# Optimization experiments

Measured on AMD Instinct MI355X. Metric: run time of the kernel, lower is better.

## Reference

```python
import jax, jax.numpy as jnp
import numpy as np

N_NODES = 50000
N_EDGES = 640000
IN_DIM = 4
EMBED = 128
OUT_DIM = 1
N_LAYERS = 3


def setup_inputs() -> dict:
    key = jax.random.key(0)
    ks = jax.random.split(key, 12)
    node_feats = jax.random.normal(ks[0], (N_NODES, IN_DIM), dtype=jnp.float32)
    src = jax.random.randint(ks[1], (N_EDGES,), 0, N_NODES, dtype=jnp.int64 if jax.config.x64_enabled else jnp.int32)
    dst = jax.random.randint(ks[2], (N_EDGES,), 0, N_NODES, dtype=jnp.int64 if jax.config.x64_enabled else jnp.int32)
    s = 1.0 / np.sqrt(EMBED)
    W_emb = jax.random.normal(ks[3], (IN_DIM, EMBED), dtype=jnp.float32) * (1.0 / np.sqrt(IN_DIM))
    b_emb = jnp.zeros((EMBED,), dtype=jnp.float32)
    W_g = jax.random.normal(ks[4], (N_LAYERS, EMBED, EMBED), dtype=jnp.float32) * s
    b_g = jnp.zeros((N_LAYERS, EMBED), dtype=jnp.float32)
    W_o1 = jax.random.normal(ks[5], (EMBED, EMBED), dtype=jnp.float32) * s
    b_o1 = jnp.zeros((EMBED,), dtype=jnp.float32)
    W_o2 = jax.random.normal(ks[6], (EMBED, OUT_DIM), dtype=jnp.float32) * s
    b_o2 = jnp.zeros((OUT_DIM,), dtype=jnp.float32)
    return {"node_feats": node_feats, "src": src, "dst": dst,
            "W_emb": W_emb, "b_emb": b_emb, "W_g": W_g, "b_g": b_g,
            "W_o1": W_o1, "b_o1": b_o1, "W_o2": W_o2, "b_o2": b_o2}


def reference(node_feats, src, dst, W_emb, b_emb, W_g, b_g, W_o1, b_o1, W_o2, b_o2):
    n = node_feats.shape[0]
    ones = jnp.ones(src.shape[0], dtype=node_feats.dtype)
    # DGL GraphConv norm='both': symmetric degree normalization, degrees clamped to >=1
    out_deg = jnp.clip(jax.ops.segment_sum(ones, src, num_segments=n), 1.0)
    in_deg = jnp.clip(jax.ops.segment_sum(ones, dst, num_segments=n), 1.0)
    norm_src = (out_deg ** -0.5)[:, None]  # [N,1]
    norm_dst = (in_deg ** -0.5)[:, None]   # [N,1]

    h = node_feats @ W_emb + b_emb  # [N, E]
    for l in range(W_g.shape[0]):
        x = h * norm_src                                        # scale sources
        agg = jax.ops.segment_sum(x[src], dst, num_segments=n)  # SpMM gather/scatter
        h = agg * norm_dst
        h = h @ W_g[l] + b_g[l]
        h = jax.nn.relu(h)
    h = jax.nn.relu(h @ W_o1 + b_o1)
    return h @ W_o2 + b_o2  # [N, out_dim]
```

## Files before the change

kernel.cpp:

```cpp
#include <hip/hip_runtime.h>

#define NN 50000
#define NE 640000
#define NPAD 50176
#define SCAN_B 196

typedef short bf16x8 __attribute__((ext_vector_type(8)));
typedef float f32x4 __attribute__((ext_vector_type(4)));

__device__ __forceinline__ unsigned short f2bf(float f) {
  unsigned int u = __float_as_uint(f);
  unsigned int r = (u + 0x7FFFu + ((u >> 16) & 1u)) >> 16;
  return (unsigned short)r;
}
__device__ __forceinline__ float bf2f(unsigned short h) {
  return __uint_as_float(((unsigned int)h) << 16);
}

typedef const __attribute__((address_space(1))) void* gptr_t;
typedef __attribute__((address_space(3))) void* lptr_t;
__device__ __forceinline__ void gload16(const void* g, void* l) {
  __builtin_amdgcn_global_load_lds((gptr_t)g, (lptr_t)l, 16, 0, 0);
}

__global__ __launch_bounds__(256) void k_deg(const int* __restrict__ src,
                                             const int* __restrict__ dst,
                                             int* __restrict__ rep_out,
                                             int* __restrict__ rep_in,
                                             int* __restrict__ rank) {
  int e = blockIdx.x * 256 + threadIdx.x;
  int r = blockIdx.x & 7;
  if (e < NE) {
    atomicAdd(&rep_out[r * NPAD + src[e]], 1);
    rank[e] = atomicAdd(&rep_in[r * NPAD + dst[e]], 1);
  }
}

__global__ __launch_bounds__(256) void k_scan1(const int* __restrict__ rep_out,
                                               const int* __restrict__ rep_in,
                                               float* __restrict__ nsrc,
                                               float* __restrict__ ndst,
                                               int* __restrict__ in_cnt,
                                               int* __restrict__ repoff,
                                               int* __restrict__ bsum) {
  int t = threadIdx.x, n = blockIdx.x * 256 + t;
  int tot_in = 0;
  if (n < NN) {
    int od = 0;
#pragma unroll
    for (int r = 0; r < 8; ++r) od += rep_out[r * NPAD + n];
    int pf = 0;
#pragma unroll
    for (int r = 0; r < 8; ++r) {
      repoff[n * 8 + r] = pf;
      pf += rep_in[r * NPAD + n];
    }
    tot_in = pf;
    in_cnt[n] = tot_in;
    nsrc[n] = 1.0f / sqrtf((float)max(od, 1));
    ndst[n] = 1.0f / sqrtf((float)max(tot_in, 1));
  }
  int s = tot_in;
#pragma unroll
  for (int o = 32; o >= 1; o >>= 1) s += __shfl_down(s, o);
  __shared__ int ws4[4];
  if ((t & 63) == 0) ws4[t >> 6] = s;
  __syncthreads();
  if (t == 0) bsum[blockIdx.x] = ws4[0] + ws4[1] + ws4[2] + ws4[3];
}

__global__ __launch_bounds__(256) void k_scan3(const int* __restrict__ in_cnt,
                                               const int* __restrict__ bsum,
                                               int* __restrict__ row_start) {
  int b = blockIdx.x, t = threadIdx.x, lane = t & 63, w = t >> 6;
  __shared__ int wtot[4];
  __shared__ int sbase;
  {
    int v = (t < b) ? bsum[t] : 0;
#pragma unroll
    for (int o = 32; o >= 1; o >>= 1) v += __shfl_down(v, o);
    if (lane == 0) wtot[w] = v;
    __syncthreads();
    if (t == 0) sbase = wtot[0] + wtot[1] + wtot[2] + wtot[3];
    __syncthreads();
  }
  int i = b * 256 + t;
  int v = (i < NN) ? in_cnt[i] : 0;
  int sc = v;
#pragma unroll
  for (int o = 1; o < 64; o <<= 1) {
    int x = __shfl_up(sc, o);
    if (lane >= o) sc += x;
  }
  if (lane == 63) wtot[w] = sc;
  __syncthreads();
  int base = sbase;
  for (int j = 0; j < w; ++j) base += wtot[j];
  if (i < NN) row_start[i] = base + sc - v;
}

__global__ __launch_bounds__(256) void k_fill(const int* __restrict__ src,
                                              const int* __restrict__ dst,
                                              const int* __restrict__ row_start,
                                              const int* __restrict__ repoff,
                                              const int* __restrict__ rank,
                                              int* __restrict__ col) {
  int e = blockIdx.x * 256 + threadIdx.x;
  int r = blockIdx.x & 7;
  if (e < NE) {
    int d = dst[e];
    col[row_start[d] + repoff[d * 8 + r] + rank[e]] = src[e];
  }
}

__global__ __launch_bounds__(256) void k_embed_prep(const float* __restrict__ nf,
                                                    const float* __restrict__ W,
                                                    const float* __restrict__ b,
                                                    const float* __restrict__ nsrc,
                                                    float* __restrict__ xs,
                                                    const float* __restrict__ Wg,
                                                    const float* __restrict__ Wo1,
                                                    unsigned short* __restrict__ wt) {
  int bid = blockIdx.x;
  if (bid < 25000) {
    int idx = bid * 256 + threadIdx.x;
    int n = idx >> 7, j = idx & 127;
    const float* f = nf + n * 4;
    float acc = b[j];
    acc += f[0] * W[j] + f[1] * W[128 + j] + f[2] * W[256 + j] + f[3] * W[384 + j];
    xs[idx] = acc * nsrc[n];
  } else {
    int idx = (bid - 25000) * 256 + threadIdx.x;
    int mat = idx >> 14, rem = idx & 16383;
    int k = rem >> 7, n = rem & 127;
    const float* Wsrc = (mat < 3) ? (Wg + mat * 16384) : Wo1;
    float v = Wsrc[k * 128 + n];
    unsigned short hi = f2bf(v);
    float lo = v - bf2f(hi);
    unsigned short* base = wt + mat * 32768;
    base[n * 128 + k] = hi;
    base[16384 + n * 128 + k] = f2bf(lo);
  }
}

__global__ __launch_bounds__(256) void k_spmm(const float* __restrict__ xs,
                                              unsigned short* __restrict__ ahi,
                                              unsigned short* __restrict__ alo,
                                              const int* __restrict__ col,
                                              const int* __restrict__ row_start,
                                              const int* __restrict__ in_cnt,
                                              const float* __restrict__ ndst) {
  int node = blockIdx.x * 4 + (threadIdx.x >> 6);
  int lane = threadIdx.x & 63;
  int half = lane >> 5;
  int ql = lane & 31;
  int start = row_start[node];
  int cnt = in_cnt[node];
  float4 acc = make_float4(0.f, 0.f, 0.f, 0.f);
  const float4* X4 = (const float4*)xs;
  for (int base = 0; base < cnt; base += 64) {
    int m = min(cnt - base, 64);
    int ccol = (lane < m) ? col[start + base + lane] : 0;
    for (int jj = 0; jj < m; jj += 8) {
      int i0 = jj + half, i1 = i0 + 2, i2 = i0 + 4, i3 = i0 + 6;
      int mm = m - 1;
      int s0 = __shfl(ccol, min(i0, mm));
      int s1 = __shfl(ccol, min(i1, mm));
      int s2 = __shfl(ccol, min(i2, mm));
      int s3 = __shfl(ccol, min(i3, mm));
      float f0 = (i0 < m) ? 1.f : 0.f;
      float f1 = (i1 < m) ? 1.f : 0.f;
      float f2 = (i2 < m) ? 1.f : 0.f;
      float f3 = (i3 < m) ? 1.f : 0.f;
      float4 v0 = X4[(size_t)s0 * 32 + ql];
      float4 v1 = X4[(size_t)s1 * 32 + ql];
      float4 v2 = X4[(size_t)s2 * 32 + ql];
      float4 v3 = X4[(size_t)s3 * 32 + ql];
      acc.x = fmaf(f0, v0.x, acc.x); acc.y = fmaf(f0, v0.y, acc.y);
      acc.z = fmaf(f0, v0.z, acc.z); acc.w = fmaf(f0, v0.w, acc.w);
      acc.x = fmaf(f1, v1.x, acc.x); acc.y = fmaf(f1, v1.y, acc.y);
      acc.z = fmaf(f1, v1.z, acc.z); acc.w = fmaf(f1, v1.w, acc.w);
      acc.x = fmaf(f2, v2.x, acc.x); acc.y = fmaf(f2, v2.y, acc.y);
      acc.z = fmaf(f2, v2.z, acc.z); acc.w = fmaf(f2, v2.w, acc.w);
      acc.x = fmaf(f3, v3.x, acc.x); acc.y = fmaf(f3, v3.y, acc.y);
      acc.z = fmaf(f3, v3.z, acc.z); acc.w = fmaf(f3, v3.w, acc.w);
    }
  }
  acc.x += __shfl_down(acc.x, 32);
  acc.y += __shfl_down(acc.y, 32);
  acc.z += __shfl_down(acc.z, 32);
  acc.w += __shfl_down(acc.w, 32);
  if (half == 0) {
    float nd = ndst[node];
    float v0 = acc.x * nd, v1 = acc.y * nd, v2 = acc.z * nd, v3 = acc.w * nd;
    ushort4 h, l;
    h.x = f2bf(v0); l.x = f2bf(v0 - bf2f(h.x));
    h.y = f2bf(v1); l.y = f2bf(v1 - bf2f(h.y));
    h.z = f2bf(v2); l.z = f2bf(v2 - bf2f(h.z));
    h.w = f2bf(v3); l.w = f2bf(v3 - bf2f(h.w));
    *(ushort4*)(ahi + (size_t)node * 128 + ql * 4) = h;
    *(ushort4*)(alo + (size_t)node * 128 + ql * 4) = l;
  }
}

__global__ __launch_bounds__(256) void k_gemm_mfma(
    const unsigned short* __restrict__ Ahi, const unsigned short* __restrict__ Alo,
    const unsigned short* __restrict__ Wth, const unsigned short* __restrict__ Wtl,
    const float* __restrict__ bias, float* __restrict__ outf,
    unsigned short* __restrict__ outhi, unsigned short* __restrict__ outlo,
    const float* __restrict__ nsrc, const float* __restrict__ W_o2,
    const float* __restrict__ b_o2, int M, int mode) {
  __shared__ unsigned short sm[2 * 64 * 128];
  __shared__ float smred[4][64];
  int tid = threadIdx.x;
  int lane = tid & 63, w = tid >> 6;
  int tile0 = blockIdx.x * 64;

  {
    int slot = lane & 15;
#pragma unroll
    for (int j = 0; j < 4; ++j) {
      int ldsoff = w * 4096 + j * 1024;
      int row = (ldsoff >> 8) + (lane >> 4);
      int grow = tile0 + row;
      if (grow > M - 1) grow = M - 1;
      size_t gsrc = (size_t)grow * 256 + (size_t)(((slot ^ (row & 7)) << 4));
      gload16((const char*)Ahi + gsrc, (char*)sm + ldsoff);
      gload16((const char*)Alo + gsrc, (char*)sm + 16384 + ldsoff);
    }
  }

  bf16x8 bh[2][4], bl[2][4];
  {
    int koff = (lane >> 4) * 8;
#pragma unroll
    for (int cf = 0; cf < 2; ++cf) {
      int n = w * 32 + cf * 16 + (lane & 15);
      const unsigned short* ph = Wth + (size_t)n * 128 + koff;
      const unsigned short* pl = Wtl + (size_t)n * 128 + koff;
#pragma unroll
      for (int kc = 0; kc < 4; ++kc) {
        bh[cf][kc] = *(const bf16x8*)(ph + kc * 32);
        bl[cf][kc] = *(const bf16x8*)(pl + kc * 32);
      }
    }
  }

  f32x4 acc[4][2] = {};
  __syncthreads();

  int r15 = lane & 15, kq = lane >> 4;
  for (int kc = 0; kc < 4; ++kc) {
    bf16x8 ah[4], al[4];
#pragma unroll
    for (int m = 0; m < 4; ++m) {
      int row = m * 16 + r15;
      int boff = row * 256 + ((((kc * 4 + kq) ^ (row & 7))) << 4);
      ah[m] = *(const bf16x8*)((const char*)sm + boff);
      al[m] = *(const bf16x8*)((const char*)sm + 16384 + boff);
    }
#pragma unroll
    for (int m = 0; m < 4; ++m)
#pragma unroll
      for (int cf = 0; cf < 2; ++cf) {
        acc[m][cf] = __builtin_amdgcn_mfma_f32_16x16x32_bf16(ah[m], bh[cf][kc], acc[m][cf], 0, 0, 0);
        acc[m][cf] = __builtin_amdgcn_mfma_f32_16x16x32_bf16(ah[m], bl[cf][kc], acc[m][cf], 0, 0, 0);
        acc[m][cf] = __builtin_amdgcn_mfma_f32_16x16x32_bf16(al[m], bh[cf][kc], acc[m][cf], 0, 0, 0);
      }
  }

  if (mode == 3) {
    float w2v[2], bv2[2];
#pragma unroll
    for (int cf = 0; cf < 2; ++cf) {
      int colg = w * 32 + cf * 16 + r15;
      w2v[cf] = W_o2[colg];
      bv2[cf] = bias[colg];
    }
#pragma unroll
    for (int m = 0; m < 4; ++m) {
#pragma unroll
      for (int i = 0; i < 4; ++i) {
        float p = fmaxf(acc[m][0][i] + bv2[0], 0.f) * w2v[0] +
                  fmaxf(acc[m][1][i] + bv2[1], 0.f) * w2v[1];
#pragma unroll
        for (int msk = 1; msk < 16; msk <<= 1) p += __shfl_xor(p, msk);
        if (r15 == 0) smred[w][m * 16 + kq * 4 + i] = p;
      }
    }
    __syncthreads();
    if (tid < 64) {
      int gr = tile0 + tid;
      if (gr < M)
        outf[gr] = smred[0][tid] + smred[1][tid] + smred[2][tid] + smred[3][tid] + b_o2[0];
    }
    return;
  }
#pragma unroll
  for (int cf = 0; cf < 2; ++cf) {
    int colg = w * 32 + cf * 16 + r15;
    float bv = bias[colg];
#pragma unroll
    for (int m = 0; m < 4; ++m) {
#pragma unroll
      for (int i = 0; i < 4; ++i) {
        int gr = tile0 + m * 16 + kq * 4 + i;
        if (gr < M) {
          float v = fmaxf(acc[m][cf][i] + bv, 0.f);
          if (mode == 0) {
            outf[(size_t)gr * 128 + colg] = v * nsrc[gr];
          } else {
            unsigned short h = f2bf(v);
            outhi[(size_t)gr * 128 + colg] = h;
            outlo[(size_t)gr * 128 + colg] = f2bf(v - bf2f(h));
          }
        }
      }
    }
  }
}

extern "C" void kernel_launch(void* const* d_in, const int* in_sizes, int n_in,
                              void* d_out, int out_size, void* d_ws, size_t ws_size,
                              hipStream_t stream) {
  const float* node_feats = (const float*)d_in[0];
  const int* src = (const int*)d_in[1];
  const int* dst = (const int*)d_in[2];
  const float* W_emb = (const float*)d_in[3];
  const float* b_emb = (const float*)d_in[4];
  const float* W_g = (const float*)d_in[5];
  const float* b_g = (const float*)d_in[6];
  const float* W_o1 = (const float*)d_in[7];
  const float* b_o1 = (const float*)d_in[8];
  const float* W_o2 = (const float*)d_in[9];
  const float* b_o2 = (const float*)d_in[10];
  float* out = (float*)d_out;

  char* ws = (char*)d_ws;
  int* rep_out   = (int*)(ws + 0);
  int* rep_in    = (int*)(ws + 1605632);
  int* in_cnt    = (int*)(ws + 3211264);
  int* row_start = (int*)(ws + 3411968);
  float* nsrc    = (float*)(ws + 3612672);
  float* ndst    = (float*)(ws + 3813376);
  int* repoff    = (int*)(ws + 4014080);
  int* bsum      = (int*)(ws + 5619712);
  int* col       = (int*)(ws + 5620736);
  unsigned short* wt = (unsigned short*)(ws + 8180736);
  float* X       = (float*)(ws + 8442880);
  unsigned short* Xu = (unsigned short*)(ws + 8442880);
  int* rank      = (int*)(ws + 8442880);
  unsigned short* Ahi = (unsigned short*)(ws + 34042880);
  unsigned short* Alo = (unsigned short*)(ws + 46842880);

  hipMemsetAsync(d_ws, 0, 3211264, stream);

  k_deg<<<(NE + 255) / 256, 256, 0, stream>>>(src, dst, rep_out, rep_in, rank);
  k_scan1<<<SCAN_B, 256, 0, stream>>>(rep_out, rep_in, nsrc, ndst, in_cnt, repoff, bsum);
  k_scan3<<<SCAN_B, 256, 0, stream>>>(in_cnt, bsum, row_start);
  k_fill<<<(NE + 255) / 256, 256, 0, stream>>>(src, dst, row_start, repoff, rank, col);
  k_embed_prep<<<25256, 256, 0, stream>>>(node_feats, W_emb, b_emb, nsrc, X,
                                          W_g, W_o1, wt);

  int gemm_grid = (NN + 63) / 64;
  for (int l = 0; l < 3; ++l) {
    k_spmm<<<NN / 4, 256, 0, stream>>>(X, Ahi, Alo, col, row_start, in_cnt, ndst);
    unsigned short* wth = wt + l * 32768;
    unsigned short* wtl = wth + 16384;
    if (l < 2) {
      k_gemm_mfma<<<gemm_grid, 256, 0, stream>>>(Ahi, Alo, wth, wtl, b_g + l * 128,
                                                 X, nullptr, nullptr, nsrc,
                                                 nullptr, nullptr, NN, 0);
    } else {
      k_gemm_mfma<<<gemm_grid, 256, 0, stream>>>(Ahi, Alo, wth, wtl, b_g + l * 128,
                                                 nullptr, Xu, Xu + 6400000, nsrc,
                                                 nullptr, nullptr, NN, 1);
    }
  }
  k_gemm_mfma<<<gemm_grid, 256, 0, stream>>>(Xu, Xu + 6400000, wt + 3 * 32768,
                                             wt + 3 * 32768 + 16384, b_o1,
                                             out, nullptr, nullptr, nsrc,
                                             W_o2, b_o2, NN, 3);
}
```

Baseline: 390.1 us.

## Build CSR with per-block LDS histograms instead of global atomics

```diff
diff --git a/kernel.cpp b/kernel.cpp
--- a/kernel.cpp
+++ b/kernel.cpp
@@ -4,6 +4,10 @@
 #define NE 640000
 #define NPAD 50176
 #define SCAN_B 196
+#define OUT_CHUNKS 64
+#define OUT_CE 10000
+#define IN_CHUNKS 128
+#define IN_CE 5000
 
 typedef short bf16x8 __attribute__((ext_vector_type(8)));
 typedef float f32x4 __attribute__((ext_vector_type(4)));
@@ -23,37 +27,52 @@
   __builtin_amdgcn_global_load_lds((gptr_t)g, (lptr_t)l, 16, 0, 0);
 }
 
-__global__ __launch_bounds__(256) void k_deg(const int* __restrict__ src,
-                                             const int* __restrict__ dst,
-                                             int* __restrict__ rep_out,
-                                             int* __restrict__ rep_in,
-                                             int* __restrict__ rank) {
-  int e = blockIdx.x * 256 + threadIdx.x;
-  int r = blockIdx.x & 7;
-  if (e < NE) {
-    atomicAdd(&rep_out[r * NPAD + src[e]], 1);
-    rank[e] = atomicAdd(&rep_in[r * NPAD + dst[e]], 1);
-  }
-}
-
-__global__ __launch_bounds__(256) void k_scan1(const int* __restrict__ rep_out,
-                                               const int* __restrict__ rep_in,
+__global__ __launch_bounds__(256) void k_hist(const int* __restrict__ src,
+                                              const int* __restrict__ dst,
+                                              unsigned short* __restrict__ hist_out,
+                                              unsigned short* __restrict__ hist_in) {
+  __shared__ unsigned int h[NPAD / 2];
+  int b = blockIdx.x, tid = threadIdx.x;
+  for (int i = tid; i < NPAD / 2; i += 256) h[i] = 0;
+  __syncthreads();
+  if (b < OUT_CHUNKS) {
+    int base = b * OUT_CE;
+    for (int i = tid; i < OUT_CE; i += 256) {
+      int n = src[base + i];
+      atomicAdd(&h[n >> 1], (n & 1) ? 0x10000u : 1u);
+    }
+  } else {
+    int base = (b - OUT_CHUNKS) * IN_CE;
+    for (int i = tid; i < IN_CE; i += 256) {
+      int n = dst[base + i];
+      atomicAdd(&h[n >> 1], (n & 1) ? 0x10000u : 1u);
+    }
+  }
+  __syncthreads();
+  unsigned int* outp = (unsigned int*)((b < OUT_CHUNKS ? hist_out : hist_in) +
+                                       (size_t)(b < OUT_CHUNKS ? b : b - OUT_CHUNKS) * NPAD);
+  for (int i = tid; i < NPAD / 2; i += 256) outp[i] = h[i];
+}
+
+__global__ __launch_bounds__(256) void k_scan1(const unsigned short* __restrict__ hist_out,
+                                               unsigned short* __restrict__ hist_in,
                                                float* __restrict__ nsrc,
                                                float* __restrict__ ndst,
                                                int* __restrict__ in_cnt,
-                                               int* __restrict__ repoff,
                                                int* __restrict__ bsum) {
   int t = threadIdx.x, n = blockIdx.x * 256 + t;
   int tot_in = 0;
   if (n < NN) {
     int od = 0;
-#pragma unroll
-    for (int r = 0; r < 8; ++r) od += rep_out[r * NPAD + n];
+#pragma unroll 8
+    for (int c = 0; c < OUT_CHUNKS; ++c) od += hist_out[(size_t)c * NPAD + n];
     int pf = 0;
-#pragma unroll
-    for (int r = 0; r < 8; ++r) {
-      repoff[n * 8 + r] = pf;
-      pf += rep_in[r * NPAD + n];
+#pragma unroll 8
+    for (int c = 0; c < IN_CHUNKS; ++c) {
+      size_t idx = (size_t)c * NPAD + n;
+      unsigned short v = hist_in[idx];
+      hist_in[idx] = (unsigned short)pf;
+      pf += v;
     }
     tot_in = pf;
     in_cnt[n] = tot_in;
@@ -102,14 +121,18 @@
 __global__ __launch_bounds__(256) void k_fill(const int* __restrict__ src,
                                               const int* __restrict__ dst,
                                               const int* __restrict__ row_start,
-                                              const int* __restrict__ repoff,
-                                              const int* __restrict__ rank,
+                                              const unsigned short* __restrict__ prefix,
                                               int* __restrict__ col) {
-  int e = blockIdx.x * 256 + threadIdx.x;
-  int r = blockIdx.x & 7;
-  if (e < NE) {
-    int d = dst[e];
-    col[row_start[d] + repoff[d * 8 + r] + rank[e]] = src[e];
+  __shared__ unsigned int h[NPAD / 2];
+  int c = blockIdx.x, tid = threadIdx.x;
+  for (int i = tid; i < NPAD / 2; i += 256) h[i] = 0;
+  __syncthreads();
+  int base = c * IN_CE;
+  for (int i = tid; i < IN_CE; i += 256) {
+    int d = dst[base + i];
+    unsigned int old = atomicAdd(&h[d >> 1], (d & 1) ? 0x10000u : 1u);
+    int rank = (d & 1) ? (int)(old >> 16) : (int)(old & 0xFFFFu);
+    col[row_start[d] + (int)prefix[(size_t)c * NPAD + d] + rank] = src[base + i];
   }
 }
 
@@ -137,9 +160,9 @@
     float v = Wsrc[k * 128 + n];
     unsigned short hi = f2bf(v);
     float lo = v - bf2f(hi);
-    unsigned short* base = wt + mat * 32768;
-    base[n * 128 + k] = hi;
-    base[16384 + n * 128 + k] = f2bf(lo);
+    unsigned short* basep = wt + mat * 32768;
+    basep[n * 128 + k] = hi;
+    basep[16384 + n * 128 + k] = f2bf(lo);
   }
 }
 
@@ -337,28 +360,24 @@
   float* out = (float*)d_out;
 
   char* ws = (char*)d_ws;
-  int* rep_out   = (int*)(ws + 0);
-  int* rep_in    = (int*)(ws + 1605632);
-  int* in_cnt    = (int*)(ws + 3211264);
-  int* row_start = (int*)(ws + 3411968);
-  float* nsrc    = (float*)(ws + 3612672);
-  float* ndst    = (float*)(ws + 3813376);
-  int* repoff    = (int*)(ws + 4014080);
-  int* bsum      = (int*)(ws + 5619712);
-  int* col       = (int*)(ws + 5620736);
-  unsigned short* wt = (unsigned short*)(ws + 8180736);
-  float* X       = (float*)(ws + 8442880);
-  unsigned short* Xu = (unsigned short*)(ws + 8442880);
-  int* rank      = (int*)(ws + 8442880);
-  unsigned short* Ahi = (unsigned short*)(ws + 34042880);
-  unsigned short* Alo = (unsigned short*)(ws + 46842880);
-
-  hipMemsetAsync(d_ws, 0, 3211264, stream);
-
-  k_deg<<<(NE + 255) / 256, 256, 0, stream>>>(src, dst, rep_out, rep_in, rank);
-  k_scan1<<<SCAN_B, 256, 0, stream>>>(rep_out, rep_in, nsrc, ndst, in_cnt, repoff, bsum);
+  int* in_cnt    = (int*)(ws + 0);
+  int* row_start = (int*)(ws + 200704);
+  float* nsrc    = (float*)(ws + 401408);
+  float* ndst    = (float*)(ws + 602112);
+  int* bsum      = (int*)(ws + 802816);
+  int* col       = (int*)(ws + 803840);
+  unsigned short* wt = (unsigned short*)(ws + 3363840);
+  float* X       = (float*)(ws + 3625984);
+  unsigned short* Xu = (unsigned short*)(ws + 3625984);
+  unsigned short* hist_out = (unsigned short*)(ws + 3625984);
+  unsigned short* hist_in  = (unsigned short*)(ws + 3625984 + 6422528);
+  unsigned short* Ahi = (unsigned short*)(ws + 29225984);
+  unsigned short* Alo = (unsigned short*)(ws + 42025984);
+
+  k_hist<<<OUT_CHUNKS + IN_CHUNKS, 256, 0, stream>>>(src, dst, hist_out, hist_in);
+  k_scan1<<<SCAN_B, 256, 0, stream>>>(hist_out, hist_in, nsrc, ndst, in_cnt, bsum);
   k_scan3<<<SCAN_B, 256, 0, stream>>>(in_cnt, bsum, row_start);
-  k_fill<<<(NE + 255) / 256, 256, 0, stream>>>(src, dst, row_start, repoff, rank, col);
+  k_fill<<<IN_CHUNKS, 256, 0, stream>>>(src, dst, row_start, hist_in, col);
   k_embed_prep<<<25256, 256, 0, stream>>>(node_feats, W_emb, b_emb, nsrc, X,
                                           W_g, W_o1, wt);
 
```

Measured after the change: 361.6 us. 7.3% less time.
